# Performance work log

Hardware: AMD Instinct MI355X
Metric: run time of the kernel (lower is better)

The kernel has to match this reference:

```python
import jax, jax.numpy as jnp
import numpy as np

NUM_HEADS = 16
EMB_SIZE = 1024
HEAD_SIZE = 64


def setup_inputs() -> dict:
    key = jax.random.key(0)
    ks = jax.random.split(key, 9)
    H, E, D = NUM_HEADS, EMB_SIZE, HEAD_SIZE
    s = 1.0 / np.sqrt(E)
    X = jax.random.normal(ks[0], (4, 2048, E), dtype=jnp.float32)
    Wq = jax.random.uniform(ks[1], (H, E, D), jnp.float32, -s, s)
    Wk = jax.random.uniform(ks[2], (H, E, D), jnp.float32, -s, s)
    Wv = jax.random.uniform(ks[3], (H, E, D), jnp.float32, -s, s)
    bq = jax.random.uniform(ks[4], (H, D), jnp.float32, -s, s)
    bk = jax.random.uniform(ks[5], (H, D), jnp.float32, -s, s)
    bv = jax.random.uniform(ks[6], (H, D), jnp.float32, -s, s)
    so = 1.0 / np.sqrt(H * D)
    Wo = jax.random.uniform(ks[7], (H * D, E), jnp.float32, -so, so)
    bo = jax.random.uniform(ks[8], (E,), jnp.float32, -so, so)
    return {"X": X, "Wq": Wq, "Wk": Wk, "Wv": Wv, "bq": bq, "bk": bk, "bv": bv, "Wo": Wo, "bo": bo}


def reference(X, Wq, Wk, Wv, bq, bk, bv, Wo, bo):
    B, S, E = X.shape
    H, _, D = Wq.shape
    # per-head projections (batched over heads)
    q = jnp.einsum('bse,hed->bhsd', X, Wq) + bq[None, :, None, :]
    k = jnp.einsum('bse,hed->bhsd', X, Wk) + bk[None, :, None, :]
    v = jnp.einsum('bse,hed->bhsd', X, Wv) + bv[None, :, None, :]
    # causal scaled-dot-product attention
    scores = jnp.einsum('bhsd,bhtd->bhst', q, k) / jnp.sqrt(jnp.float32(D))
    causal = jnp.tril(jnp.ones((S, S), dtype=bool))
    scores = jnp.where(causal[None, None], scores, jnp.float32(-jnp.inf))
    probs = jax.nn.softmax(scores, axis=-1)
    out = jnp.einsum('bhst,bhtd->bhsd', probs, v)
    # concat heads (head h occupies slots [h*D:(h+1)*D]) then output proj
    concat = out.transpose(0, 2, 1, 3).reshape(B, S, H * D)
    # dropout is identity in eval mode
    return concat @ Wo + bo
```

## Files before the change

kernel.cpp:

```cpp
#include <hip/hip_runtime.h>
#include <stdint.h>


typedef float   f32x4  __attribute__((ext_vector_type(4)));
typedef __bf16  bf16x8 __attribute__((ext_vector_type(8)));
typedef short   short8 __attribute__((ext_vector_type(8)));
typedef unsigned short ushort4v __attribute__((ext_vector_type(4)));

typedef __attribute__((address_space(1))) void GV;
typedef __attribute__((address_space(3))) void LV;

#define DEVI static __device__ __forceinline__

DEVI unsigned short f2bf(float f){
  unsigned u = __float_as_uint(f);
  unsigned r = u + 0x7fffu + ((u>>16)&1u);
  return (unsigned short)(r>>16);
}

DEVI unsigned cvt_pk_bf16(float lo, float hi){
  unsigned r;
  asm("v_cvt_pk_bf16_f32 %0, %1, %2" : "=v"(r) : "v"(lo), "v"(hi));
  return r;
}

DEVI void gl_lds16(const void* g, void* l){
  __builtin_amdgcn_global_load_lds((GV*)g, (LV*)l, 16, 0, 0);
}

__global__ __launch_bounds__(256) void pack_x(const float* __restrict__ X,
                                              short* __restrict__ Xb){
  int i = blockIdx.x*256 + threadIdx.x;
  const float4* p = (const float4*)(X + (size_t)i*8);
  float4 a = p[0], b = p[1];
  short8 o;
  o[0]=(short)f2bf(a.x); o[1]=(short)f2bf(a.y); o[2]=(short)f2bf(a.z); o[3]=(short)f2bf(a.w);
  o[4]=(short)f2bf(b.x); o[5]=(short)f2bf(b.y); o[6]=(short)f2bf(b.z); o[7]=(short)f2bf(b.w);
  *(short8*)(Xb + (size_t)i*8) = o;
}

__global__ __launch_bounds__(256) void pack_wqkv(const float* __restrict__ Wq,
                                                 const float* __restrict__ Wk,
                                                 const float* __restrict__ Wv,
                                                 short* __restrict__ Wp){
  int t = blockIdx.x*256 + threadIdx.x;
  int n = t >> 7, kc = t & 127;
  int which = n >> 10, hd = n & 1023, h = hd >> 6, d = hd & 63;
  const float* W = which==0 ? Wq : (which==1 ? Wk : Wv);
  const float* src = W + ((size_t)h*1024 + kc*8)*64 + d;
  short8 o;
  #pragma unroll
  for (int j=0;j<8;++j) o[j] = (short)f2bf(src[(size_t)j*64]);
  *(short8*)(Wp + (size_t)n*1024 + kc*8) = o;
}

__global__ __launch_bounds__(256) void pack_wo(const float* __restrict__ Wo,
                                               short* __restrict__ WoT){
  int t = blockIdx.x*256 + threadIdx.x;
  int n = t >> 7, kc = t & 127;
  const float* src = Wo + (size_t)(kc*8)*1024 + n;
  short8 o;
  #pragma unroll
  for (int j=0;j<8;++j) o[j] = (short)f2bf(src[(size_t)j*1024]);
  *(short8*)(WoT + (size_t)n*1024 + kc*8) = o;
}

template<int MODE>
__global__ __launch_bounds__(512)
void gemm256(const short* __restrict__ A, const short* __restrict__ Bt,
             const float* __restrict__ b0, const float* __restrict__ b1,
             const float* __restrict__ b2,
             short* __restrict__ Qb, short* __restrict__ Kb, short* __restrict__ Vtb,
             float* __restrict__ Out)
{
  __shared__ __align__(16) char sm[3][49152];
  const int K2 = 2048;
  int t = threadIdx.x, lane = t & 63, wid = t >> 6;
  int wr = wid >> 2, wc = wid & 3;
  int l15 = lane & 15, l4 = lane >> 4;
  int nwg = gridDim.x, qd = nwg >> 3;
  int swz = (blockIdx.x & 7) * qd + (blockIdx.x >> 3);
  int bm = swz & 63, bn = swz >> 6;
  size_t abase = (size_t)bm * 128 * K2;
  size_t bbase = (size_t)bn * 256 * K2;

  f32x4 acc[4][4] = {};

  auto stage = [&](int kt, char* buf){
    int kb = kt * 128;
    #pragma unroll
    for (int c = 0; c < 2; ++c){
      int x = c*8192 + t*16;
      int r = x >> 7, z = x & 127;
      int zs = z ^ ((r & 7) << 4);
      gl_lds16((const char*)A + abase + (size_t)r*K2 + kb + zs, buf + c*8192 + wid*1024);
    }
    #pragma unroll
    for (int c = 0; c < 4; ++c){
      int x = c*8192 + t*16;
      int r = x >> 7, z = x & 127;
      int zs = z ^ ((r & 7) << 4);
      gl_lds16((const char*)Bt + bbase + (size_t)r*K2 + kb + zs, buf + 16384 + c*8192 + wid*1024);
    }
  };

  auto compute = [&](const char* buf){
    const char* sA = buf;
    const char* sB = buf + 16384;
    #pragma unroll
    for (int kk = 0; kk < 2; ++kk){
      bf16x8 af[4], bfr[4];
      int cb = kk*64 + l4*16;
      #pragma unroll
      for (int i = 0; i < 4; ++i){
        int ra = wr*64 + i*16 + l15;
        af[i]  = *(const bf16x8*)(sA + ra*128 + (cb ^ ((ra&7)<<4)));
        int rb = wc*64 + i*16 + l15;
        bfr[i] = *(const bf16x8*)(sB + rb*128 + (cb ^ ((rb&7)<<4)));
      }
      __builtin_amdgcn_s_setprio(1);
      #pragma unroll
      for (int i = 0; i < 4; ++i)
        #pragma unroll
        for (int j = 0; j < 4; ++j)
          acc[i][j] = __builtin_amdgcn_mfma_f32_16x16x32_bf16(af[i], bfr[j], acc[i][j], 0, 0, 0);
      __builtin_amdgcn_s_setprio(0);
    }
  };

  stage(0, sm[0]);
  stage(1, sm[1]);
  for (int kt = 0; kt < 14; ++kt){
    stage(kt + 2, sm[(kt + 2) % 3]);
    asm volatile("s_waitcnt vmcnt(12)\n\ts_barrier" ::: "memory");
    compute(sm[kt % 3]);
    asm volatile("s_barrier" ::: "memory");
  }
  asm volatile("s_waitcnt vmcnt(6)\n\ts_barrier" ::: "memory");
  compute(sm[2]);
  asm volatile("s_waitcnt vmcnt(0)" ::: "memory");
  compute(sm[0]);

  #pragma unroll
  for (int i = 0; i < 4; ++i){
    int mbase = bm*128 + wr*64 + i*16 + l4*4;
    #pragma unroll
    for (int j = 0; j < 4; ++j){
      int n = bn*256 + wc*64 + j*16 + l15;
      if (MODE == 0){
        int which = n >> 10, hd = n & 1023, h = hd >> 6, d = hd & 63;
        const float* bp = which==0 ? b0 : (which==1 ? b1 : b2);
        float bias = bp[hd];
        int b = mbase >> 11, sbase = mbase & 2047;
        size_t bh = (size_t)(b*16 + h);
        if (which == 2){
          ushort4v pv;
          #pragma unroll
          for (int r = 0; r < 4; ++r) pv[r] = f2bf(acc[i][j][r] + bias);
          *(ushort4v*)(Vtb + (bh*64 + d)*2048 + sbase) = pv;
        } else {
          short* dst = (which==0 ? Qb : Kb) + bh*2048*64;
          float sc = which==0 ? 0.18033688f : 1.0f;
          #pragma unroll
          for (int r = 0; r < 4; ++r)
            dst[(size_t)(sbase + r)*64 + d] = (short)f2bf((acc[i][j][r] + bias) * sc);
        }
      } else {
        float bias = b0[n];
        #pragma unroll
        for (int r = 0; r < 4; ++r)
          Out[(size_t)(mbase + r)*1024 + n] = acc[i][j][r] + bias;
      }
    }
  }
}

__global__ __launch_bounds__(256, 4)
void attn(const short* __restrict__ Qb, const short* __restrict__ Kb,
          const short* __restrict__ Vtb, short* __restrict__ Ob)
{
  __shared__ __align__(16) char smK[2][8192];
  __shared__ __align__(16) char smV[2][8192];
  __shared__ __align__(16) char smP[4][2048];
  int t = threadIdx.x, lane = t & 63, wid = t >> 6;
  int l15 = lane & 15, hi = lane >> 4;
  int hi16 = hi*16, hi4 = hi*4;
  int bh = blockIdx.x & 63;
  int j = blockIdx.x >> 6;
  int qb = (j < 8) ? (15 - j) : (j - 8);
  int b = bh >> 4, h = bh & 15;
  int q0 = qb * 128;
  int wq0 = q0 + wid * 32;
  const char* Qh = (const char*)(Qb + (size_t)bh*2048*64);
  const char* Kh = (const char*)(Kb + (size_t)bh*2048*64);
  const char* Vh = (const char*)(Vtb + (size_t)bh*64*2048);
  char* Pw = smP[wid];

  bf16x8 vones;
  #pragma unroll
  for (int z = 0; z < 8; ++z) vones[z] = (__bf16)1.0f;

  bf16x8 qf[2][2];
  #pragma unroll
  for (int qt = 0; qt < 2; ++qt)
    #pragma unroll
    for (int kk = 0; kk < 2; ++kk)
      qf[qt][kk] = *(const bf16x8*)(Qh + (size_t)(wq0 + qt*16 + l15)*128 + kk*64 + hi16);

  f32x4 oacc[2][4] = {};
  f32x4 lacc[2] = {};
  float m[2] = {-1e30f, -1e30f};

  int nkt = 2*qb + 2;

  #pragma unroll
  for (int c = 0; c < 2; ++c){
    int x = c*4096 + t*16;
    int r = x >> 7, z = x & 127;
    int zs = z ^ ((r & 7) << 4);
    gl_lds16(Kh + (size_t)r*128 + zs, smK[0] + c*4096 + wid*1024);
    gl_lds16(Vh + (size_t)r*4096 + zs, smV[0] + c*4096 + wid*1024);
  }
  __syncthreads();

  for (int kt = 0; kt < nkt; ++kt){
    int cur = kt & 1;
    if (kt + 1 < nkt){
      int nxt = cur ^ 1;
      #pragma unroll
      for (int c = 0; c < 2; ++c){
        int x = c*4096 + t*16;
        int r = x >> 7, z = x & 127;
        int zs = z ^ ((r & 7) << 4);
        gl_lds16(Kh + (size_t)(kt+1)*8192 + (size_t)r*128 + zs, smK[nxt] + c*4096 + wid*1024);
        gl_lds16(Vh + (size_t)r*4096 + (size_t)(kt+1)*128 + zs, smV[nxt] + c*4096 + wid*1024);
      }
    }
    const char* Kc = smK[cur];
    const char* Vc = smV[cur];
    int kbase = kt * 64;

    #pragma unroll
    for (int qt = 0; qt < 2; ++qt){
      int qlo = wq0 + qt*16;
      if (kbase > qlo + 15) continue;

      f32x4 sa[4];
      __builtin_amdgcn_s_setprio(1);
      #pragma unroll
      for (int nt = 0; nt < 4; ++nt){
        f32x4 a = {};
        #pragma unroll
        for (int kk = 0; kk < 2; ++kk){
          int rk = nt*16 + l15;
          bf16x8 kf = *(const bf16x8*)(Kc + rk*128 + ((kk*64 + hi16) ^ ((rk&7)<<4)));
          a = __builtin_amdgcn_mfma_f32_16x16x32_bf16(kf, qf[qt][kk], a, 0, 0, 0);
        }
        sa[nt] = a;
      }
      __builtin_amdgcn_s_setprio(0);

      int qrow = qlo + l15;
      if (kbase + 63 > qlo){
        #pragma unroll
        for (int nt = 0; nt < 4; ++nt)
          #pragma unroll
          for (int r = 0; r < 4; ++r)
            if (kbase + nt*16 + hi4 + r > qrow) sa[nt][r] = -1e30f;
      }

      float pm;
      {
        float t0 = fmaxf(fmaxf(sa[0][0], sa[0][1]), sa[0][2]);
        float t1 = fmaxf(fmaxf(sa[0][3], sa[1][0]), sa[1][1]);
        float t2 = fmaxf(fmaxf(sa[1][2], sa[1][3]), sa[2][0]);
        float t3 = fmaxf(fmaxf(sa[2][1], sa[2][2]), sa[2][3]);
        float t4 = fmaxf(fmaxf(sa[3][0], sa[3][1]), sa[3][2]);
        float u0 = fmaxf(fmaxf(t0, t1), sa[3][3]);
        float u1 = fmaxf(fmaxf(t2, t3), t4);
        pm = fmaxf(u0, u1);
      }
      pm = fmaxf(pm, __shfl_xor(pm, 16));
      pm = fmaxf(pm, __shfl_xor(pm, 32));
      float mq = m[qt];
      if (!__all(pm <= mq + 8.0f)){
        float mnew = fmaxf(mq, pm);
        float sc = exp2f(mq - mnew);
        lacc[qt] *= sc;
        #pragma unroll
        for (int dt = 0; dt < 4; ++dt) oacc[qt][dt] *= sc;
        m[qt] = mnew; mq = mnew;
      }
      unsigned pw[8];
      #pragma unroll
      for (int nt = 0; nt < 4; ++nt){
        float p0 = exp2f(sa[nt][0] - mq);
        float p1 = exp2f(sa[nt][1] - mq);
        float p2 = exp2f(sa[nt][2] - mq);
        float p3 = exp2f(sa[nt][3] - mq);
        pw[nt*2]   = cvt_pk_bf16(p0, p1);
        pw[nt*2+1] = cvt_pk_bf16(p2, p3);
      }

      {
        char* base = Pw + l15*128;
        int sw = (l15 & 7) << 4;
        #pragma unroll
        for (int nt = 0; nt < 4; ++nt){
          unsigned long long w = (unsigned long long)pw[nt*2] |
                                 ((unsigned long long)pw[nt*2+1] << 32);
          *(unsigned long long*)(base + ((nt*32 + hi*8) ^ sw)) = w;
        }
      }

      __builtin_amdgcn_s_setprio(1);
      #pragma unroll
      for (int kk = 0; kk < 2; ++kk){
        bf16x8 pf = *(const bf16x8*)(Pw + l15*128 + ((kk*64 + hi16) ^ ((l15&7)<<4)));
        lacc[qt] = __builtin_amdgcn_mfma_f32_16x16x32_bf16(vones, pf, lacc[qt], 0, 0, 0);
        #pragma unroll
        for (int dt = 0; dt < 4; ++dt){
          int rv = dt*16 + l15;
          bf16x8 vf = *(const bf16x8*)(Vc + rv*128 + ((kk*64 + hi16) ^ ((rv&7)<<4)));
          oacc[qt][dt] = __builtin_amdgcn_mfma_f32_16x16x32_bf16(vf, pf, oacc[qt][dt], 0, 0, 0);
        }
      }
      __builtin_amdgcn_s_setprio(0);
    }
    __syncthreads();
  }

  #pragma unroll
  for (int qt = 0; qt < 2; ++qt){
    float inv = 1.0f / lacc[qt][0];
    int srow = wq0 + qt*16 + l15;
    size_t rb = ((size_t)(b*2048 + srow))*1024 + h*64 + hi4;
    #pragma unroll
    for (int dt = 0; dt < 4; ++dt){
      unsigned w0 = cvt_pk_bf16(oacc[qt][dt][0]*inv, oacc[qt][dt][1]*inv);
      unsigned w1 = cvt_pk_bf16(oacc[qt][dt][2]*inv, oacc[qt][dt][3]*inv);
      *(unsigned long long*)(Ob + rb + dt*16) =
          ((unsigned long long)w1 << 32) | (unsigned long long)w0;
    }
  }
}

extern "C" void kernel_launch(void* const* d_in, const int* in_sizes, int n_in,
                              void* d_out, int out_size, void* d_ws, size_t ws_size,
                              hipStream_t stream)
{
  const float* X  = (const float*)d_in[0];
  const float* Wq = (const float*)d_in[1];
  const float* Wk = (const float*)d_in[2];
  const float* Wv = (const float*)d_in[3];
  const float* bq = (const float*)d_in[4];
  const float* bk = (const float*)d_in[5];
  const float* bv = (const float*)d_in[6];
  const float* Wo = (const float*)d_in[7];
  const float* bo = (const float*)d_in[8];
  float* Out = (float*)d_out;

  char* ws = (char*)d_ws;
  short* Xbf  = (short*)(ws);
  short* Wp   = (short*)(ws + 16777216);
  short* WoT  = (short*)(ws + 23068672);
  short* Qb   = (short*)(ws + 25165824);
  short* Kb   = (short*)(ws + 41943040);
  short* Vtb  = (short*)(ws + 58720256);
  short* Ob   = (short*)(ws + 75497472);

  pack_x   <<<4096, 256, 0, stream>>>(X, Xbf);
  pack_wqkv<<<1536, 256, 0, stream>>>(Wq, Wk, Wv, Wp);
  pack_wo  <<< 512, 256, 0, stream>>>(Wo, WoT);

  gemm256<0><<<768, 512, 0, stream>>>(Xbf, Wp, bq, bk, bv, Qb, Kb, Vtb, nullptr);
  attn      <<<64*16, 256, 0, stream>>>(Qb, Kb, Vtb, Ob);
  gemm256<1><<<256, 512, 0, stream>>>(Ob, WoT, bo, nullptr, nullptr,
                                      nullptr, nullptr, nullptr, Out);
}
```

Before: 204.5 us.

## Shrink attention Q tile to 64 rows and pass P via permlane swaps

The attention kernel now gives each block 64 query rows (16 per wave) instead of 128, launches 2048 blocks ordered heaviest-first, and raises the occupancy hint to 5 blocks per CU. The softmax probabilities are rearranged into MFMA B-operand layout in registers with v_permlane32/16_swap, so the per-wave shared-memory P round trip is gone. This aims at better load balance and less LDS traffic and register pressure. In exchange, each K/V tile loaded into LDS now serves half as many query rows, which raises global and LDS load traffic per unit of work.

```diff
diff --git a/kernel.cpp b/kernel.cpp
--- a/kernel.cpp
+++ b/kernel.cpp
@@ -22,6 +22,13 @@
   unsigned r;
   asm("v_cvt_pk_bf16_f32 %0, %1, %2" : "=v"(r) : "v"(lo), "v"(hi));
   return r;
+}
+
+DEVI void permlane32_swap(unsigned &a, unsigned &b){
+  asm volatile("v_permlane32_swap_b32 %0, %1" : "+v"(a), "+v"(b));
+}
+DEVI void permlane16_swap(unsigned &a, unsigned &b){
+  asm volatile("v_permlane16_swap_b32 %0, %1" : "+v"(a), "+v"(b));
 }
 
 DEVI void gl_lds16(const void* g, void* l){
@@ -175,43 +182,37 @@
   }
 }
 
-__global__ __launch_bounds__(256, 4)
+__global__ __launch_bounds__(256, 5)
 void attn(const short* __restrict__ Qb, const short* __restrict__ Kb,
           const short* __restrict__ Vtb, short* __restrict__ Ob)
 {
   __shared__ __align__(16) char smK[2][8192];
   __shared__ __align__(16) char smV[2][8192];
-  __shared__ __align__(16) char smP[4][2048];
   int t = threadIdx.x, lane = t & 63, wid = t >> 6;
   int l15 = lane & 15, hi = lane >> 4;
   int hi16 = hi*16, hi4 = hi*4;
   int bh = blockIdx.x & 63;
-  int j = blockIdx.x >> 6;
-  int qb = (j < 8) ? (15 - j) : (j - 8);
+  int qb = 31 - (blockIdx.x >> 6);
   int b = bh >> 4, h = bh & 15;
-  int q0 = qb * 128;
-  int wq0 = q0 + wid * 32;
+  int wq0 = qb*64 + wid*16;
   const char* Qh = (const char*)(Qb + (size_t)bh*2048*64);
   const char* Kh = (const char*)(Kb + (size_t)bh*2048*64);
   const char* Vh = (const char*)(Vtb + (size_t)bh*64*2048);
-  char* Pw = smP[wid];
 
   bf16x8 vones;
   #pragma unroll
   for (int z = 0; z < 8; ++z) vones[z] = (__bf16)1.0f;
 
-  bf16x8 qf[2][2];
-  #pragma unroll
-  for (int qt = 0; qt < 2; ++qt)
-    #pragma unroll
-    for (int kk = 0; kk < 2; ++kk)
-      qf[qt][kk] = *(const bf16x8*)(Qh + (size_t)(wq0 + qt*16 + l15)*128 + kk*64 + hi16);
-
-  f32x4 oacc[2][4] = {};
-  f32x4 lacc[2] = {};
-  float m[2] = {-1e30f, -1e30f};
-
-  int nkt = 2*qb + 2;
+  bf16x8 qf[2];
+  #pragma unroll
+  for (int kk = 0; kk < 2; ++kk)
+    qf[kk] = *(const bf16x8*)(Qh + (size_t)(wq0 + l15)*128 + kk*64 + hi16);
+
+  f32x4 oacc[4] = {};
+  f32x4 lacc = {};
+  float m = -1e30f;
+
+  int nkt = qb + 1;
 
   #pragma unroll
   for (int c = 0; c < 2; ++c){
@@ -240,108 +241,102 @@
     const char* Vc = smV[cur];
     int kbase = kt * 64;
 
-    #pragma unroll
-    for (int qt = 0; qt < 2; ++qt){
-      int qlo = wq0 + qt*16;
-      if (kbase > qlo + 15) continue;
-
-      f32x4 sa[4];
-      __builtin_amdgcn_s_setprio(1);
-      #pragma unroll
-      for (int nt = 0; nt < 4; ++nt){
-        f32x4 a = {};
+    f32x4 sa[4];
+    __builtin_amdgcn_s_setprio(1);
+    #pragma unroll
+    for (int nt = 0; nt < 4; ++nt){
+      f32x4 a = {};
+      #pragma unroll
+      for (int kk = 0; kk < 2; ++kk){
+        int rk = nt*16 + l15;
+        bf16x8 kf = *(const bf16x8*)(Kc + rk*128 + ((kk*64 + hi16) ^ ((rk&7)<<4)));
+        a = __builtin_amdgcn_mfma_f32_16x16x32_bf16(kf, qf[kk], a, 0, 0, 0);
+      }
+      sa[nt] = a;
+    }
+    __builtin_amdgcn_s_setprio(0);
+
+    if (kt == qb){
+      int qrow = wq0 + l15;
+      #pragma unroll
+      for (int nt = 0; nt < 4; ++nt)
         #pragma unroll
-        for (int kk = 0; kk < 2; ++kk){
-          int rk = nt*16 + l15;
-          bf16x8 kf = *(const bf16x8*)(Kc + rk*128 + ((kk*64 + hi16) ^ ((rk&7)<<4)));
-          a = __builtin_amdgcn_mfma_f32_16x16x32_bf16(kf, qf[qt][kk], a, 0, 0, 0);
-        }
-        sa[nt] = a;
-      }
-      __builtin_amdgcn_s_setprio(0);
-
-      int qrow = qlo + l15;
-      if (kbase + 63 > qlo){
-        #pragma unroll
-        for (int nt = 0; nt < 4; ++nt)
-          #pragma unroll
-          for (int r = 0; r < 4; ++r)
-            if (kbase + nt*16 + hi4 + r > qrow) sa[nt][r] = -1e30f;
-      }
-
-      float pm;
-      {
-        float t0 = fmaxf(fmaxf(sa[0][0], sa[0][1]), sa[0][2]);
-        float t1 = fmaxf(fmaxf(sa[0][3], sa[1][0]), sa[1][1]);
-        float t2 = fmaxf(fmaxf(sa[1][2], sa[1][3]), sa[2][0]);
-        float t3 = fmaxf(fmaxf(sa[2][1], sa[2][2]), sa[2][3]);
-        float t4 = fmaxf(fmaxf(sa[3][0], sa[3][1]), sa[3][2]);
-        float u0 = fmaxf(fmaxf(t0, t1), sa[3][3]);
-        float u1 = fmaxf(fmaxf(t2, t3), t4);
-        pm = fmaxf(u0, u1);
-      }
-      pm = fmaxf(pm, __shfl_xor(pm, 16));
-      pm = fmaxf(pm, __shfl_xor(pm, 32));
-      float mq = m[qt];
-      if (!__all(pm <= mq + 8.0f)){
-        float mnew = fmaxf(mq, pm);
-        float sc = exp2f(mq - mnew);
-        lacc[qt] *= sc;
-        #pragma unroll
-        for (int dt = 0; dt < 4; ++dt) oacc[qt][dt] *= sc;
-        m[qt] = mnew; mq = mnew;
-      }
-      unsigned pw[8];
-      #pragma unroll
-      for (int nt = 0; nt < 4; ++nt){
-        float p0 = exp2f(sa[nt][0] - mq);
-        float p1 = exp2f(sa[nt][1] - mq);
-        float p2 = exp2f(sa[nt][2] - mq);
-        float p3 = exp2f(sa[nt][3] - mq);
-        pw[nt*2]   = cvt_pk_bf16(p0, p1);
-        pw[nt*2+1] = cvt_pk_bf16(p2, p3);
-      }
-
-      {
-        char* base = Pw + l15*128;
-        int sw = (l15 & 7) << 4;
-        #pragma unroll
-        for (int nt = 0; nt < 4; ++nt){
-          unsigned long long w = (unsigned long long)pw[nt*2] |
-                                 ((unsigned long long)pw[nt*2+1] << 32);
-          *(unsigned long long*)(base + ((nt*32 + hi*8) ^ sw)) = w;
-        }
-      }
-
-      __builtin_amdgcn_s_setprio(1);
-      #pragma unroll
-      for (int kk = 0; kk < 2; ++kk){
-        bf16x8 pf = *(const bf16x8*)(Pw + l15*128 + ((kk*64 + hi16) ^ ((l15&7)<<4)));
-        lacc[qt] = __builtin_amdgcn_mfma_f32_16x16x32_bf16(vones, pf, lacc[qt], 0, 0, 0);
-        #pragma unroll
-        for (int dt = 0; dt < 4; ++dt){
-          int rv = dt*16 + l15;
-          bf16x8 vf = *(const bf16x8*)(Vc + rv*128 + ((kk*64 + hi16) ^ ((rv&7)<<4)));
-          oacc[qt][dt] = __builtin_amdgcn_mfma_f32_16x16x32_bf16(vf, pf, oacc[qt][dt], 0, 0, 0);
-        }
-      }
-      __builtin_amdgcn_s_setprio(0);
-    }
+        for (int r = 0; r < 4; ++r)
+          if (kbase + nt*16 + hi4 + r > qrow) sa[nt][r] = -1e30f;
+    }
+
+    float pm;
+    {
+      float t0 = fmaxf(fmaxf(sa[0][0], sa[0][1]), sa[0][2]);
+      float t1 = fmaxf(fmaxf(sa[0][3], sa[1][0]), sa[1][1]);
+      float t2 = fmaxf(fmaxf(sa[1][2], sa[1][3]), sa[2][0]);
+      float t3 = fmaxf(fmaxf(sa[2][1], sa[2][2]), sa[2][3]);
+      float t4 = fmaxf(fmaxf(sa[3][0], sa[3][1]), sa[3][2]);
+      float u0 = fmaxf(fmaxf(t0, t1), sa[3][3]);
+      float u1 = fmaxf(fmaxf(t2, t3), t4);
+      pm = fmaxf(u0, u1);
+    }
+    pm = fmaxf(pm, __shfl_xor(pm, 16));
+    pm = fmaxf(pm, __shfl_xor(pm, 32));
+    if (!__all(pm <= m + 8.0f)){
+      float mnew = fmaxf(m, pm);
+      float sc = exp2f(m - mnew);
+      lacc *= sc;
+      #pragma unroll
+      for (int dt = 0; dt < 4; ++dt) oacc[dt] *= sc;
+      m = mnew;
+    }
+    unsigned pw[8];
+    #pragma unroll
+    for (int nt = 0; nt < 4; ++nt){
+      float p0 = exp2f(sa[nt][0] - m);
+      float p1 = exp2f(sa[nt][1] - m);
+      float p2 = exp2f(sa[nt][2] - m);
+      float p3 = exp2f(sa[nt][3] - m);
+      pw[nt*2]   = cvt_pk_bf16(p0, p1);
+      pw[nt*2+1] = cvt_pk_bf16(p2, p3);
+    }
+
+    union U { unsigned u[4]; bf16x8 v; } f0, f1;
+    {
+      unsigned a0 = pw[0], b0v = pw[2];
+      permlane32_swap(a0, b0v); permlane16_swap(a0, b0v);
+      unsigned a1 = pw[1], b1v = pw[3];
+      permlane32_swap(a1, b1v); permlane16_swap(a1, b1v);
+      f0.u[0] = a0; f0.u[1] = a1; f0.u[2] = b0v; f0.u[3] = b1v;
+      unsigned a2 = pw[4], b2v = pw[6];
+      permlane32_swap(a2, b2v); permlane16_swap(a2, b2v);
+      unsigned a3 = pw[5], b3v = pw[7];
+      permlane32_swap(a3, b3v); permlane16_swap(a3, b3v);
+      f1.u[0] = a2; f1.u[1] = a3; f1.u[2] = b2v; f1.u[3] = b3v;
+    }
+
+    __builtin_amdgcn_s_setprio(1);
+    #pragma unroll
+    for (int kk = 0; kk < 2; ++kk){
+      bf16x8 pf = kk ? f1.v : f0.v;
+      lacc = __builtin_amdgcn_mfma_f32_16x16x32_bf16(vones, pf, lacc, 0, 0, 0);
+      #pragma unroll
+      for (int dt = 0; dt < 4; ++dt){
+        int rv = dt*16 + l15;
+        bf16x8 vf = *(const bf16x8*)(Vc + rv*128 + ((kk*64 + hi16) ^ ((rv&7)<<4)));
+        oacc[dt] = __builtin_amdgcn_mfma_f32_16x16x32_bf16(vf, pf, oacc[dt], 0, 0, 0);
+      }
+    }
+    __builtin_amdgcn_s_setprio(0);
+
     __syncthreads();
   }
 
-  #pragma unroll
-  for (int qt = 0; qt < 2; ++qt){
-    float inv = 1.0f / lacc[qt][0];
-    int srow = wq0 + qt*16 + l15;
-    size_t rb = ((size_t)(b*2048 + srow))*1024 + h*64 + hi4;
-    #pragma unroll
-    for (int dt = 0; dt < 4; ++dt){
-      unsigned w0 = cvt_pk_bf16(oacc[qt][dt][0]*inv, oacc[qt][dt][1]*inv);
-      unsigned w1 = cvt_pk_bf16(oacc[qt][dt][2]*inv, oacc[qt][dt][3]*inv);
-      *(unsigned long long*)(Ob + rb + dt*16) =
-          ((unsigned long long)w1 << 32) | (unsigned long long)w0;
-    }
+  float inv = 1.0f / lacc[0];
+  int srow = wq0 + l15;
+  size_t rb = ((size_t)(b*2048 + srow))*1024 + h*64 + hi4;
+  #pragma unroll
+  for (int dt = 0; dt < 4; ++dt){
+    unsigned w0 = cvt_pk_bf16(oacc[dt][0]*inv, oacc[dt][1]*inv);
+    unsigned w1 = cvt_pk_bf16(oacc[dt][2]*inv, oacc[dt][3]*inv);
+    *(unsigned long long*)(Ob + rb + dt*16) =
+        ((unsigned long long)w1 << 32) | (unsigned long long)w0;
   }
 }
 
@@ -374,7 +369,7 @@
   pack_wo  <<< 512, 256, 0, stream>>>(Wo, WoT);
 
   gemm256<0><<<768, 512, 0, stream>>>(Xbf, Wp, bq, bk, bv, Qb, Kb, Vtb, nullptr);
-  attn      <<<64*16, 256, 0, stream>>>(Qb, Kb, Vtb, Ob);
+  attn      <<<2048, 256, 0, stream>>>(Qb, Kb, Vtb, Ob);
   gemm256<1><<<256, 512, 0, stream>>>(Ob, WoT, bo, nullptr, nullptr,
                                       nullptr, nullptr, nullptr, Out);
 }
```

New measurement: 196.7 us. -3.8%, faster.
